# Optimization experiments

Hardware: AMD Instinct MI355X
Metric: run time of the kernel (lower is better)

Reference implementation:

```python
import jax, jax.numpy as jnp
import numpy as np

B = 4096; NINP = 512; NHID = 2048; NB = 8; BS = 256  # block_size_out
ATT_OUT = 4 * BS; TOPK = 4; DK_I = 64; NH = 4; DK_M = 16


def setup_inputs() -> dict:
    ks = jax.random.split(jax.random.key(0), 16)
    g = lambda i, shape, s=0.01: s * jax.random.normal(ks[i], shape, dtype=jnp.float32)
    return dict(
        inp=jax.random.normal(ks[0], (B, NINP), dtype=jnp.float32),
        hx=jax.random.normal(ks[1], (B, NHID), dtype=jnp.float32),
        cx=jax.random.normal(ks[2], (B, NHID), dtype=jnp.float32),
        # inp_att group-linear projections (GroupLinearLayer init 0.01*randn)
        Wq_i=g(3, (NB, BS, DK_I)), Wk_i=g(4, (2, NINP, DK_I)), Wv_i=g(5, (2, NINP, ATT_OUT)),
        # mha group-linear projections (4 heads * d_k=16)
        Wq_m=g(6, (NB, BS, NH * DK_M)), Wk_m=g(7, (NB, BS, NH * DK_M)), Wv_m=g(8, (NB, BS, NH * DK_M)),
        fc_w=g(9, (BS, NH * DK_M), 0.05), fc_b=jnp.zeros((BS,), jnp.float32),
        gate_w=g(10, (BS, NH * DK_M), 0.05), gate_b=jnp.zeros((BS,), jnp.float32),
        # blockified LSTMCell: k=NB independent (ATT_OUT -> BS) cells, gate order i,f,g,o
        Wih=g(11, (NB, 4 * BS, ATT_OUT), 0.02), Whh=g(12, (NB, 4 * BS, BS), 0.05),
        b_ih=jnp.zeros((NB, 4 * BS), jnp.float32), b_hh=jnp.zeros((NB, 4 * BS), jnp.float32),
        step=0,
    )


def _fwd(inp, hx, cx, Wq_i, Wk_i, Wv_i, Wq_m, Wk_m, Wv_m, fc_w, fc_b, gate_w, gate_b, Wih, Whh, b_ih, b_hh):
    b = inp.shape[0]
    # input read: concat null slot + input (num_blocks_in=1, num_modules_read_input=2)
    x = inp.reshape(b, 1, NINP)
    x = jnp.concatenate([jnp.zeros_like(x), x], axis=1)  # (b, 2, NINP); slot 0 = null
    hq = hx.reshape(b, NB, BS)
    q = jnp.einsum('bkd,kde->bke', hq, Wq_i)              # (b, NB, DK_I)
    k = jnp.einsum('bkd,kde->bke', x, Wk_i)               # (b, 2, DK_I)
    v = jnp.einsum('bkd,kde->bke', x, Wv_i)               # (b, 2, ATT_OUT)
    iatt = jax.nn.softmax(jnp.einsum('bqe,bke->bqk', q, k) / jnp.sqrt(jnp.float32(DK_I)), axis=-1)
    inp_use = jnp.einsum('bqk,bke->bqe', iatt, v)         # (b, NB, ATT_OUT); skip_write => identity fc
    # top-k selection: blocks with HIGHEST null-attention get frozen (masked out)
    _, botk = jax.lax.top_k(iatt[:, :, 0], NB - TOPK)
    mblk = jnp.ones((b, NB), inp.dtype).at[jnp.arange(b)[:, None], botk].set(0.0)
    mblk = jax.lax.stop_gradient(mblk)                    # mask.detach()
    mask = jnp.repeat(mblk, BS, axis=1)                   # (b, NHID)
    # block-diagonal LSTM cell (post blockify_params)
    hb = hx.reshape(b, NB, BS); cb = cx.reshape(b, NB, BS)
    gates = jnp.einsum('bkd,kgd->bkg', inp_use, Wih) + jnp.einsum('bkh,kgh->bkg', hb, Whh) + b_ih + b_hh
    ig, fg, gg, og = jnp.split(gates, 4, axis=-1)
    c_new = jax.nn.sigmoid(fg) * cb + jax.nn.sigmoid(ig) * jnp.tanh(gg)
    h_new = jax.nn.sigmoid(og) * jnp.tanh(c_new)          # (b, NB, BS)
    # step attention among blocks; blocked_grad: forward identity, backward masked
    m3 = mblk[:, :, None]
    hg = m3 * h_new + jax.lax.stop_gradient((1.0 - m3) * h_new)
    qm = jnp.einsum('bkd,kde->bke', hg, Wq_m).reshape(b, NB, NH, DK_M)
    km = jnp.einsum('bkd,kde->bke', hg, Wk_m).reshape(b, NB, NH, DK_M)
    vm = jnp.einsum('bkd,kde->bke', hg, Wv_m).reshape(b, NB, NH, DK_M)
    a = jax.nn.softmax(jnp.einsum('bqhe,bkhe->bhqk', qm, km) / jnp.sqrt(jnp.float32(DK_M)), axis=-1)
    o = jnp.einsum('bhqk,bkhe->bqhe', a, vm).reshape(b, NB, NH * DK_M)
    att_out = jax.nn.sigmoid(o @ gate_w.T + gate_b) * jnp.tanh(o @ fc_w.T + fc_b)  # residual gating
    h_new = (h_new + att_out).reshape(b, NHID)
    c_new = c_new.reshape(b, NHID)
    hx_out = mask * h_new + (1.0 - mask) * hx
    cx_out = mask * c_new + (1.0 - mask) * cx
    return hx_out, cx_out, mask


def reference(inp, hx, cx, Wq_i, Wk_i, Wv_i, Wq_m, Wk_m, Wv_m, fc_w, fc_b, gate_w, gate_b, Wih, Whh, b_ih, b_hh, step):
    return _fwd(inp, hx, cx, Wq_i, Wk_i, Wv_i, Wq_m, Wk_m, Wv_m, fc_w, fc_b, gate_w, gate_b, Wih, Whh, b_ih, b_hh)
```

## Files before the change

### kernel.cpp

```cpp
#include <hip/hip_runtime.h>
#include <hip/hip_bf16.h>


#define B_SZ 4096
#define NINP 512
#define NHID 2048
#define NB 8
#define BSZ 256
#define ATT_OUT 1024

typedef __attribute__((ext_vector_type(8))) short bf16x8;
typedef __attribute__((ext_vector_type(8))) unsigned short u16x8;
typedef __attribute__((ext_vector_type(4))) float f32x4;

__device__ __forceinline__ float sigf(float x) { return 1.0f / (1.0f + expf(-x)); }

__device__ __forceinline__ unsigned short f2bf(float x) {
    unsigned u = __float_as_uint(x);
    unsigned r = (u + 0x7fff + ((u >> 16) & 1)) >> 16;
    return (unsigned short)r;
}
__device__ __forceinline__ float bf2f(unsigned short u) {
    return __uint_as_float((unsigned)u << 16);
}

__device__ __forceinline__ void gload16(const void* g, void* l) {
    __builtin_amdgcn_global_load_lds(
        (const __attribute__((address_space(1))) unsigned int*)(unsigned long long)g,
        (__attribute__((address_space(3))) unsigned int*)(unsigned int)(unsigned long long)l,
        16, 0, 0);
}

__device__ __forceinline__ u16x8 cvt8(const float4& a, const float4& b) {
    u16x8 v;
    v[0] = f2bf(a.x); v[1] = f2bf(a.y); v[2] = f2bf(a.z); v[3] = f2bf(a.w);
    v[4] = f2bf(b.x); v[5] = f2bf(b.y); v[6] = f2bf(b.z); v[7] = f2bf(b.w);
    return v;
}

__global__ __launch_bounds__(256) void prep1_kernel(
    const float* __restrict__ gw, const float* __restrict__ fw,
    unsigned short* __restrict__ Wgfb,
    const float4* __restrict__ hx4, u16x8* __restrict__ hxb8,
    const float4* __restrict__ inp4, u16x8* __restrict__ inpb8,
    const float* __restrict__ WvSrc, unsigned short* __restrict__ Wvb)
{
    __shared__ float tile[32][33];
    const int bid = blockIdx.x;
    if (bid < 128) {
        int t = bid * 256 + threadIdx.x;
        Wgfb[t] = f2bf((t < 16384) ? gw[t] : fw[t - 16384]);
    } else if (bid < 4224) {
        long i = (long)(bid - 128) * 256 + threadIdx.x;
        hxb8[i] = cvt8(hx4[i * 2], hx4[i * 2 + 1]);
    } else if (bid < 5248) {
        long i = (long)(bid - 4224) * 256 + threadIdx.x;
        inpb8[i] = cvt8(inp4[i * 2], inp4[i * 2 + 1]);
    } else {
        const int b2 = bid - 5248;
        const int n0 = (b2 & 31) * 32;
        const int k0 = (b2 >> 5) * 32;
        const int tx = threadIdx.x & 31;
        const int ty = threadIdx.x >> 5;
        #pragma unroll
        for (int r = 0; r < 4; ++r)
            tile[ty + r * 8][tx] = WvSrc[(long)(k0 + ty + r * 8) * 1024 + n0 + tx];
        __syncthreads();
        #pragma unroll
        for (int r = 0; r < 4; ++r)
            Wvb[(long)(n0 + ty + r * 8) * 512 + k0 + tx] = f2bf(tile[tx][ty + r * 8]);
    }
}

__global__ __launch_bounds__(256) void prepW_kernel(
    const float4* __restrict__ Wih4, u16x8* __restrict__ Wihb8,
    const float4* __restrict__ Whh4, u16x8* __restrict__ Whhb8)
{
    const int bid = blockIdx.x;
    if (bid < 4096) {
        long i = (long)bid * 256 + threadIdx.x;
        Wihb8[i] = cvt8(Wih4[i * 2], Wih4[i * 2 + 1]);
    } else {
        long i = (long)(bid - 4096) * 256 + threadIdx.x;
        Whhb8[i] = cvt8(Whh4[i * 2], Whh4[i * 2 + 1]);
    }
}

__global__ __launch_bounds__(256) void qkvw_kernel(
    const float* __restrict__ Wq, const float* __restrict__ Wk,
    const float* __restrict__ Wv, unsigned short* __restrict__ out)
{
    int idx = blockIdx.x * 256 + threadIdx.x;
    int k = idx & 255;
    int n = (idx >> 8) % 192;
    int kb = idx / (192 * 256);
    const float* src = (n < 64) ? Wq : (n < 128) ? Wk : Wv;
    int nn = n & 63;
    out[idx] = f2bf(src[(long)kb * 16384 + k * 64 + nn]);
}

__global__ __launch_bounds__(256) void qk1_kernel(
    const float* __restrict__ inp, const float* __restrict__ hx,
    const float* __restrict__ Wk1, const float* __restrict__ Wq,
    float* __restrict__ k1, float* __restrict__ q)
{
    const int role = blockIdx.y;
    const int m0 = blockIdx.x * 64;
    const float* A; long lda; const float* Bw; int K; float* C; int ldc;
    if (role == 8) {
        A = inp + (long)m0 * 512; lda = 512; Bw = Wk1; K = 512;
        C = k1 + (long)m0 * 64; ldc = 64;
    } else {
        A = hx + (long)m0 * 2048 + role * 256; lda = 2048;
        Bw = Wq + (long)role * 256 * 64; K = 256;
        C = q + (long)m0 * 512 + role * 64; ldc = 512;
    }

    __shared__ float As[64][17];
    __shared__ float Bs[16][65];

    const int t = threadIdx.x;
    const int ty = t >> 4;
    const int tx = t & 15;

    float acc[4][4] = {};

    for (int k0 = 0; k0 < K; k0 += 16) {
        {
            int m = t >> 2, kk = (t & 3) << 2;
            float4 av = *reinterpret_cast<const float4*>(&A[(long)m * lda + k0 + kk]);
            As[m][kk] = av.x; As[m][kk + 1] = av.y;
            As[m][kk + 2] = av.z; As[m][kk + 3] = av.w;
        }
        {
            int kr = t >> 4, c = (t & 15) << 2;
            float4 bv = *reinterpret_cast<const float4*>(&Bw[(long)(k0 + kr) * 64 + c]);
            Bs[kr][c] = bv.x; Bs[kr][c + 1] = bv.y;
            Bs[kr][c + 2] = bv.z; Bs[kr][c + 3] = bv.w;
        }
        __syncthreads();
        #pragma unroll
        for (int kk = 0; kk < 16; ++kk) {
            float a[4], b[4];
            #pragma unroll
            for (int i = 0; i < 4; ++i) a[i] = As[ty * 4 + i][kk];
            #pragma unroll
            for (int j = 0; j < 4; ++j) b[j] = Bs[kk][tx * 4 + j];
            #pragma unroll
            for (int i = 0; i < 4; ++i)
                #pragma unroll
                for (int j = 0; j < 4; ++j) acc[i][j] += a[i] * b[j];
        }
        __syncthreads();
    }
    #pragma unroll
    for (int i = 0; i < 4; ++i) {
        float4 v = {acc[i][0], acc[i][1], acc[i][2], acc[i][3]};
        *reinterpret_cast<float4*>(&C[(long)(ty * 4 + i) * ldc + tx * 4]) = v;
    }
}

__global__ __launch_bounds__(256, 2) void gemm_mfma_bf(
    const unsigned short* __restrict__ A,
    const unsigned short* __restrict__ Bm,
    unsigned short* __restrict__ Cv,
    int K, int lda, int ldb, int ldc,
    long aOffZ, long bOffZ, long cOffZ)
{
    const int m0 = blockIdx.x * 128;
    const int n0 = blockIdx.y * 64;
    const int z = blockIdx.z;
    A += (long)z * aOffZ;
    Bm += (long)z * bOffZ;

    __shared__ unsigned short As[128 * 64];
    __shared__ unsigned short Bs[64 * 64];

    const int t = threadIdx.x;
    const int wid = t >> 6;
    const int l = t & 63;
    const int l15 = l & 15;
    const int l4 = l >> 4;
    const int wm = wid >> 1;
    const int wn = wid & 1;

    f32x4 acc[4][2];
    #pragma unroll
    for (int m = 0; m < 4; ++m)
        #pragma unroll
        for (int n = 0; n < 2; ++n)
            acc[m][n] = (f32x4){0.f, 0.f, 0.f, 0.f};

    for (int k0 = 0; k0 < K; k0 += 64) {
        #pragma unroll
        for (int s = 0; s < 4; ++s) {
            int ci = (wid * 4 + s) * 64 + l;
            int r = ci >> 3, cs = ci & 7;
            gload16(A + (long)(m0 + r) * lda + k0 + ((cs ^ (r & 7)) << 3), &As[ci * 8]);
        }
        #pragma unroll
        for (int s = 0; s < 2; ++s) {
            int ci = (wid * 2 + s) * 64 + l;
            int rn = ci >> 3, cs = ci & 7;
            gload16(Bm + (long)(n0 + rn) * ldb + k0 + ((cs ^ (rn & 7)) << 3), &Bs[ci * 8]);
        }
        __syncthreads();
        #pragma unroll
        for (int kh = 0; kh < 2; ++kh) {
            bf16x8 af[4];
            #pragma unroll
            for (int m = 0; m < 4; ++m) {
                int r = wm * 64 + m * 16 + l15;
                int c = kh * 4 + l4;
                af[m] = *reinterpret_cast<const bf16x8*>(&As[r * 64 + ((c ^ (r & 7)) << 3)]);
            }
            #pragma unroll
            for (int nf = 0; nf < 2; ++nf) {
                int rn = wn * 32 + nf * 16 + l15;
                int c = kh * 4 + l4;
                bf16x8 bf = *reinterpret_cast<const bf16x8*>(
                    &Bs[rn * 64 + ((c ^ (rn & 7)) << 3)]);
                #pragma unroll
                for (int m = 0; m < 4; ++m)
                    acc[m][nf] = __builtin_amdgcn_mfma_f32_16x16x32_bf16(
                        af[m], bf, acc[m][nf], 0, 0, 0);
            }
        }
        __syncthreads();
    }

    #pragma unroll
    for (int nf = 0; nf < 2; ++nf) {
        const int ccol = n0 + wn * 32 + nf * 16 + l15;
        #pragma unroll
        for (int m = 0; m < 4; ++m) {
            #pragma unroll
            for (int r = 0; r < 4; ++r) {
                const long crow = m0 + wm * 64 + m * 16 + l4 * 4 + r;
                Cv[(long)z * cOffZ + crow * ldc + ccol] = f2bf(acc[m][nf][r]);
            }
        }
    }
}

__global__ __launch_bounds__(256) void s1_mask_kernel(
    const float* __restrict__ q, const float* __restrict__ k1,
    float* __restrict__ w_ws, float* __restrict__ mblk,
    float* __restrict__ mask_out)
{
    const int wave = threadIdx.x >> 6;
    const int lane = threadIdx.x & 63;
    const int b = blockIdx.x * 4 + wave;

    float p[8];
    const float kv = k1[(long)b * 64 + lane];
    #pragma unroll
    for (int kb = 0; kb < 8; ++kb)
        p[kb] = q[(long)b * 512 + kb * 64 + lane] * kv;

    #pragma unroll
    for (int off = 1; off < 64; off <<= 1) {
        #pragma unroll
        for (int kb = 0; kb < 8; ++kb) p[kb] += __shfl_xor(p[kb], off);
    }

    float s[8], mv[8];
    #pragma unroll
    for (int kb = 0; kb < 8; ++kb) s[kb] = p[kb] * 0.125f;

    #pragma unroll
    for (int j = 0; j < 8; ++j) {
        int r = 0;
        #pragma unroll
        for (int i = 0; i < 8; ++i)
            r += (s[i] < s[j]) || (s[i] == s[j] && i < j);
        mv[j] = (r >= 4) ? 1.0f : 0.0f;
    }
    if (lane < 8) {
        w_ws[(long)b * 8 + lane] = sigf(s[lane]);
        mblk[(long)b * 8 + lane] = mv[lane];
    }
    #pragma unroll
    for (int it = 0; it < 8; ++it) {
        const float mvv = mv[it];
        float4 v = {mvv, mvv, mvv, mvv};
        *reinterpret_cast<float4*>(&mask_out[(long)b * 2048 + it * 256 + lane * 4]) = v;
    }
}

__global__ __launch_bounds__(256, 2) void gates_mfma_kernel(
    const unsigned short* __restrict__ Ab,
    const unsigned short* __restrict__ Hb,
    const unsigned short* __restrict__ Wihb,
    const unsigned short* __restrict__ Whhb,
    const float* __restrict__ b_ih, const float* __restrict__ b_hh,
    const float* __restrict__ w_ws, const float* __restrict__ mblk,
    const float* __restrict__ cx,
    float* __restrict__ h_out, float* __restrict__ c_out,
    unsigned short* __restrict__ hn_b)
{
    const int m0 = blockIdx.x * 128;
    const int j0 = blockIdx.y * 64;
    const int kb = blockIdx.z;

    __shared__ unsigned short As[128 * 64];
    __shared__ unsigned short Bs[256 * 64];
    __shared__ float wv[128];
    __shared__ float mbs[128];

    const int t = threadIdx.x;
    const int wid = t >> 6;
    const int l = t & 63;
    const int l15 = l & 15;
    const int l4 = l >> 4;
    const int wm = wid >> 1;
    const int wj = wid & 1;

    if (t < 128) {
        wv[t] = w_ws[(long)(m0 + t) * 8 + kb];
        mbs[t] = mblk[(long)(m0 + t) * 8 + kb];
    }

    f32x4 acc[4][8];
    #pragma unroll
    for (int m = 0; m < 4; ++m)
        #pragma unroll
        for (int n = 0; n < 8; ++n)
            acc[m][n] = (f32x4){0.f, 0.f, 0.f, 0.f};

    auto stage = [&](const unsigned short* Aptr, long lda,
                     const unsigned short* Bptr, long ldb, int k0) {
        #pragma unroll
        for (int s = 0; s < 4; ++s) {
            int ci = (wid * 4 + s) * 64 + l;
            int r = ci >> 3, cs = ci & 7;
            const unsigned short* g = Aptr + (long)r * lda + k0 + ((cs ^ (r & 7)) << 3);
            gload16(g, &As[ci * 8]);
        }
        #pragma unroll
        for (int s = 0; s < 8; ++s) {
            int ci = (wid * 8 + s) * 64 + l;
            int rn = ci >> 3, cs = ci & 7;
            int sg = rn >> 6, jl = rn & 63;
            const unsigned short* g = Bptr + (long)(sg * 256 + j0 + jl) * ldb + k0
                                      + ((cs ^ (rn & 7)) << 3);
            gload16(g, &Bs[ci * 8]);
        }
    };

    auto compute = [&]() {
        #pragma unroll
        for (int kh = 0; kh < 2; ++kh) {
            bf16x8 af[4];
            #pragma unroll
            for (int m = 0; m < 4; ++m) {
                int r = wm * 64 + m * 16 + l15;
                int c = kh * 4 + l4;
                af[m] = *reinterpret_cast<const bf16x8*>(&As[r * 64 + ((c ^ (r & 7)) << 3)]);
            }
            #pragma unroll
            for (int sg = 0; sg < 4; ++sg) {
                #pragma unroll
                for (int jf = 0; jf < 2; ++jf) {
                    int rn = sg * 64 + wj * 32 + jf * 16 + l15;
                    int c = kh * 4 + l4;
                    bf16x8 bf = *reinterpret_cast<const bf16x8*>(
                        &Bs[rn * 64 + ((c ^ (rn & 7)) << 3)]);
                    #pragma unroll
                    for (int m = 0; m < 4; ++m)
                        acc[m][sg * 2 + jf] = __builtin_amdgcn_mfma_f32_16x16x32_bf16(
                            af[m], bf, acc[m][sg * 2 + jf], 0, 0, 0);
                }
            }
        }
    };

    {
        const unsigned short* A1 = Ab + (long)m0 * 1024;
        const unsigned short* B1 = Wihb + (long)kb * 1024 * 1024;
        for (int k0 = 0; k0 < 1024; k0 += 64) {
            stage(A1, 1024, B1, 1024, k0);
            __syncthreads();
            compute();
            __syncthreads();
        }
    }

    {
        float wsc[4][4];
        #pragma unroll
        for (int m = 0; m < 4; ++m)
            #pragma unroll
            for (int r = 0; r < 4; ++r)
                wsc[m][r] = wv[wm * 64 + m * 16 + l4 * 4 + r];
        #pragma unroll
        for (int m = 0; m < 4; ++m)
            #pragma unroll
            for (int n = 0; n < 8; ++n)
                #pragma unroll
                for (int r = 0; r < 4; ++r)
                    acc[m][n][r] *= wsc[m][r];
    }

    {
        const unsigned short* A2 = Hb + (long)m0 * 2048 + kb * 256;
        const unsigned short* B2 = Whhb + (long)kb * 1024 * 256;
        for (int k0 = 0; k0 < 256; k0 += 64) {
            stage(A2, 2048, B2, 256, k0);
            __syncthreads();
            compute();
            __syncthreads();
        }
    }

    #pragma unroll
    for (int jf = 0; jf < 2; ++jf) {
        const int jcol = j0 + wj * 32 + jf * 16 + l15;
        const long bb = (long)kb * 1024 + jcol;
        const float bI = b_ih[bb] + b_hh[bb];
        const float bF = b_ih[bb + 256] + b_hh[bb + 256];
        const float bG = b_ih[bb + 512] + b_hh[bb + 512];
        const float bO = b_ih[bb + 768] + b_hh[bb + 768];
        #pragma unroll
        for (int m = 0; m < 4; ++m) {
            #pragma unroll
            for (int r = 0; r < 4; ++r) {
                const long row = m0 + wm * 64 + m * 16 + l4 * 4 + r;
                const long idx = row * 2048 + kb * 256 + jcol;
                const float mv = mbs[wm * 64 + m * 16 + l4 * 4 + r];
                const float ig = acc[m][0 + jf][r] + bI;
                const float fg = acc[m][2 + jf][r] + bF;
                const float gg = acc[m][4 + jf][r] + bG;
                const float og = acc[m][6 + jf][r] + bO;
                const float co = cx[idx];
                const float cn = sigf(fg) * co + sigf(ig) * tanhf(gg);
                const float hn = sigf(og) * tanhf(cn);
                h_out[idx] = hn;
                c_out[idx] = (mv != 0.0f) ? cn : co;
                hn_b[idx] = f2bf(hn);
            }
        }
    }
}

__global__ __launch_bounds__(256) void attn_m2_kernel(
    const unsigned short* __restrict__ qkv, unsigned short* __restrict__ ob)
{
    const int tid = blockIdx.x * 256 + threadIdx.x;
    const int b = tid >> 5;
    const int qkb = (tid >> 2) & 7;
    const int h = tid & 3;
    const unsigned short* base = qkv + (long)b * 1536;

    float qv[16];
    {
        const unsigned short* qp = base + qkb * 192 + h * 16;
        #pragma unroll
        for (int e = 0; e < 16; ++e) qv[e] = bf2f(qp[e]);
    }

    float sc[8];
    float mx = -1e30f;
    #pragma unroll
    for (int kk = 0; kk < 8; ++kk) {
        const unsigned short* kp = base + kk * 192 + 64 + h * 16;
        float s = 0.f;
        #pragma unroll
        for (int e = 0; e < 16; ++e) s += qv[e] * bf2f(kp[e]);
        s *= 0.25f;
        sc[kk] = s;
        mx = fmaxf(mx, s);
    }
    float den = 0.f;
    #pragma unroll
    for (int kk = 0; kk < 8; ++kk) { sc[kk] = expf(sc[kk] - mx); den += sc[kk]; }
    const float inv = 1.0f / den;

    float ov[16] = {};
    #pragma unroll
    for (int kk = 0; kk < 8; ++kk) {
        const float pw = sc[kk] * inv;
        const unsigned short* vp = base + kk * 192 + 128 + h * 16;
        #pragma unroll
        for (int e = 0; e < 16; ++e) ov[e] += pw * bf2f(vp[e]);
    }
    u16x8 r0, r1;
    #pragma unroll
    for (int e = 0; e < 8; ++e) { r0[e] = f2bf(ov[e]); r1[e] = f2bf(ov[e + 8]); }
    unsigned short* op = ob + (long)((b * 8 + qkb) * 64 + h * 16);
    *reinterpret_cast<u16x8*>(op) = r0;
    *reinterpret_cast<u16x8*>(op + 8) = r1;
}

__global__ __launch_bounds__(256) void attn_final_kernel(
    const unsigned short* __restrict__ ob,
    const unsigned short* __restrict__ Wgfb,
    const float* __restrict__ gate_b, const float* __restrict__ fc_b,
    const float* __restrict__ mblk,
    const float* __restrict__ hx,
    float* __restrict__ h_out)
{
    const int m0 = blockIdx.x * 128;
    const int j0 = blockIdx.y * 64;

    __shared__ unsigned short As[128 * 64];
    __shared__ unsigned short Bs[128 * 64];

    const int t = threadIdx.x;
    const int wid = t >> 6;
    const int l = t & 63;
    const int l15 = l & 15;
    const int l4 = l >> 4;
    const int wm = wid >> 1;
    const int wn = wid & 1;

    #pragma unroll
    for (int s = 0; s < 4; ++s) {
        int ci = (wid * 4 + s) * 64 + l;
        int r = ci >> 3, cs = ci & 7;
        gload16(ob + (long)(m0 + r) * 64 + ((cs ^ (r & 7)) << 3), &As[ci * 8]);
    }
    #pragma unroll
    for (int s = 0; s < 4; ++s) {
        int ci = (wid * 4 + s) * 64 + l;
        int r = ci >> 3, cs = ci & 7;
        int n = (r < 64) ? (j0 + r) : (256 + j0 + (r - 64));
        gload16(Wgfb + (long)n * 64 + ((cs ^ (r & 7)) << 3), &Bs[ci * 8]);
    }
    __syncthreads();

    f32x4 acc[4][2][2];
    #pragma unroll
    for (int m = 0; m < 4; ++m)
        #pragma unroll
        for (int nf = 0; nf < 2; ++nf)
            #pragma unroll
            for (int gf = 0; gf < 2; ++gf)
                acc[m][nf][gf] = (f32x4){0.f, 0.f, 0.f, 0.f};

    #pragma unroll
    for (int kh = 0; kh < 2; ++kh) {
        const int c = kh * 4 + l4;
        bf16x8 af[4];
        #pragma unroll
        for (int m = 0; m < 4; ++m) {
            int r = wm * 64 + m * 16 + l15;
            af[m] = *reinterpret_cast<const bf16x8*>(&As[r * 64 + ((c ^ (r & 7)) << 3)]);
        }
        #pragma unroll
        for (int nf = 0; nf < 2; ++nf) {
            int rg = wn * 32 + nf * 16 + l15;
            bf16x8 bg = *reinterpret_cast<const bf16x8*>(
                &Bs[rg * 64 + ((c ^ (rg & 7)) << 3)]);
            int rf = 64 + rg;
            bf16x8 bfv = *reinterpret_cast<const bf16x8*>(
                &Bs[rf * 64 + ((c ^ (rf & 7)) << 3)]);
            #pragma unroll
            for (int m = 0; m < 4; ++m) {
                acc[m][nf][0] = __builtin_amdgcn_mfma_f32_16x16x32_bf16(
                    af[m], bg, acc[m][nf][0], 0, 0, 0);
                acc[m][nf][1] = __builtin_amdgcn_mfma_f32_16x16x32_bf16(
                    af[m], bfv, acc[m][nf][1], 0, 0, 0);
            }
        }
    }

    #pragma unroll
    for (int nf = 0; nf < 2; ++nf) {
        const int j = j0 + wn * 32 + nf * 16 + l15;
        const float gb = gate_b[j];
        const float fb = fc_b[j];
        #pragma unroll
        for (int m = 0; m < 4; ++m) {
            #pragma unroll
            for (int r = 0; r < 4; ++r) {
                const long p = m0 + wm * 64 + m * 16 + l4 * 4 + r;
                const float g = acc[m][nf][0][r] + gb;
                const float f = acc[m][nf][1][r] + fb;
                const float att = sigf(g) * tanhf(f);
                const long idx = (p >> 3) * 2048 + (p & 7) * 256 + j;
                const float mv = mblk[p];
                const float hn = h_out[idx] + att;
                h_out[idx] = (mv != 0.0f) ? hn : hx[idx];
            }
        }
    }
}

extern "C" void kernel_launch(void* const* d_in, const int* in_sizes, int n_in,
                              void* d_out, int out_size, void* d_ws, size_t ws_size,
                              hipStream_t stream) {
    const float* inp    = (const float*)d_in[0];
    const float* hx     = (const float*)d_in[1];
    const float* cx     = (const float*)d_in[2];
    const float* Wq_i   = (const float*)d_in[3];
    const float* Wk_i   = (const float*)d_in[4];
    const float* Wv_i   = (const float*)d_in[5];
    const float* Wq_m   = (const float*)d_in[6];
    const float* Wk_m   = (const float*)d_in[7];
    const float* Wv_m   = (const float*)d_in[8];
    const float* fc_w   = (const float*)d_in[9];
    const float* fc_b   = (const float*)d_in[10];
    const float* gate_w = (const float*)d_in[11];
    const float* gate_b = (const float*)d_in[12];
    const float* Wih    = (const float*)d_in[13];
    const float* Whh    = (const float*)d_in[14];
    const float* b_ih   = (const float*)d_in[15];
    const float* b_hh   = (const float*)d_in[16];

    float* out      = (float*)d_out;
    float* h_out    = out;
    float* c_out    = out + (long)B_SZ * 2048;
    float* mask_out = out + (long)2 * B_SZ * 2048;

    float* ws   = (float*)d_ws;
    float* w_ws = ws;
    float* mblk = w_ws + (long)B_SZ * 8;
    unsigned short* v1b = (unsigned short*)(mblk + (long)B_SZ * 8);
    unsigned short* hxb = v1b + (long)B_SZ * 1024;
    unsigned short* hnb  = hxb + (long)B_SZ * 2048;
    unsigned short* Wihb = hnb + (long)B_SZ * 2048;
    unsigned short* Whhb = Wihb + (long)8 * 1024 * 1024;
    unsigned short* Wgfb = Whhb + (long)8 * 1024 * 256;
    float* k1 = (float*)Wihb;
    float* q  = k1 + (long)B_SZ * 64;
    unsigned short* inpb = (unsigned short*)(q + (long)B_SZ * 512);
    unsigned short* Wvb  = inpb + (long)B_SZ * 512;
    unsigned short* Wqkvb = Wihb;
    unsigned short* qkvb  = hxb;
    unsigned short* ob    = v1b;

    prep1_kernel<<<dim3(5760), 256, 0, stream>>>(
        gate_w, fc_w, Wgfb,
        (const float4*)hx, (u16x8*)hxb,
        (const float4*)inp, (u16x8*)inpb,
        Wv_i + (long)NINP * ATT_OUT, Wvb);
    qk1_kernel<<<dim3(64, 9), 256, 0, stream>>>(
        inp, hx, Wk_i + (long)NINP * 64, Wq_i, k1, q);
    gemm_mfma_bf<<<dim3(32, 16, 1), 256, 0, stream>>>(
        inpb, Wvb, v1b, 512, 512, 512, 1024, 0, 0, 0);
    s1_mask_kernel<<<dim3(B_SZ / 4), 256, 0, stream>>>(q, k1, w_ws, mblk, mask_out);
    prepW_kernel<<<dim3(5120), 256, 0, stream>>>(
        (const float4*)Wih, (u16x8*)Wihb, (const float4*)Whh, (u16x8*)Whhb);
    gates_mfma_kernel<<<dim3(B_SZ / 128, 4, 8), 256, 0, stream>>>(
        v1b, hxb, Wihb, Whhb, b_ih, b_hh, w_ws, mblk, cx, h_out, c_out, hnb);
    qkvw_kernel<<<dim3(1536), 256, 0, stream>>>(Wq_m, Wk_m, Wv_m, Wqkvb);
    gemm_mfma_bf<<<dim3(32, 3, 8), 256, 0, stream>>>(
        hnb, Wqkvb, qkvb, 256, 2048, 256, 1536, 256, (long)192 * 256, 192);
    attn_m2_kernel<<<dim3(B_SZ * 32 / 256), 256, 0, stream>>>(qkvb, ob);
    attn_final_kernel<<<dim3(256, 4), 256, 0, stream>>>(
        ob, Wgfb, gate_b, fc_b, mblk, hx, h_out);
}
```

Baseline: 288.0 us.

## Drop fp32 h_out round trip, remap gates blocks, enlarge qk1 tiles

The gates kernel no longer writes fp32 h_new to h_out. The final attention kernel now reads the bf16 hn buffer instead, which removes a 32 MB fp32 write and a 32 MB fp32 read. The gates grid is remapped so consecutive workgroups fall on different kb blocks, likely to spread L2/XCD traffic. qk1 now uses 128-row tiles with 8x4 accumulators per thread. Reading h_new from bf16 lowers the precision of the residual add in the output.

```diff
diff --git a/kernel.cpp b/kernel.cpp
--- a/kernel.cpp
+++ b/kernel.cpp
@@ -105,7 +105,7 @@
     float* __restrict__ k1, float* __restrict__ q)
 {
     const int role = blockIdx.y;
-    const int m0 = blockIdx.x * 64;
+    const int m0 = blockIdx.x * 128;
     const float* A; long lda; const float* Bw; int K; float* C; int ldc;
     if (role == 8) {
         A = inp + (long)m0 * 512; lda = 512; Bw = Wk1; K = 512;
@@ -116,18 +116,20 @@
         C = q + (long)m0 * 512 + role * 64; ldc = 512;
     }
 
-    __shared__ float As[64][17];
+    __shared__ float As[128][17];
     __shared__ float Bs[16][65];
 
     const int t = threadIdx.x;
     const int ty = t >> 4;
     const int tx = t & 15;
 
-    float acc[4][4] = {};
+    float acc[8][4] = {};
 
     for (int k0 = 0; k0 < K; k0 += 16) {
-        {
-            int m = t >> 2, kk = (t & 3) << 2;
+        #pragma unroll
+        for (int u = 0; u < 2; ++u) {
+            int slot = t + 256 * u;
+            int m = slot >> 2, kk = (slot & 3) << 2;
             float4 av = *reinterpret_cast<const float4*>(&A[(long)m * lda + k0 + kk]);
             As[m][kk] = av.x; As[m][kk + 1] = av.y;
             As[m][kk + 2] = av.z; As[m][kk + 3] = av.w;
@@ -141,22 +143,22 @@
         __syncthreads();
         #pragma unroll
         for (int kk = 0; kk < 16; ++kk) {
-            float a[4], b[4];
-            #pragma unroll
-            for (int i = 0; i < 4; ++i) a[i] = As[ty * 4 + i][kk];
+            float a[8], b[4];
+            #pragma unroll
+            for (int i = 0; i < 8; ++i) a[i] = As[ty * 8 + i][kk];
             #pragma unroll
             for (int j = 0; j < 4; ++j) b[j] = Bs[kk][tx * 4 + j];
             #pragma unroll
-            for (int i = 0; i < 4; ++i)
+            for (int i = 0; i < 8; ++i)
                 #pragma unroll
                 for (int j = 0; j < 4; ++j) acc[i][j] += a[i] * b[j];
         }
         __syncthreads();
     }
     #pragma unroll
-    for (int i = 0; i < 4; ++i) {
+    for (int i = 0; i < 8; ++i) {
         float4 v = {acc[i][0], acc[i][1], acc[i][2], acc[i][3]};
-        *reinterpret_cast<float4*>(&C[(long)(ty * 4 + i) * ldc + tx * 4]) = v;
+        *reinterpret_cast<float4*>(&C[(long)(ty * 8 + i) * ldc + tx * 4]) = v;
     }
 }
 
@@ -296,12 +298,14 @@
     const float* __restrict__ b_ih, const float* __restrict__ b_hh,
     const float* __restrict__ w_ws, const float* __restrict__ mblk,
     const float* __restrict__ cx,
-    float* __restrict__ h_out, float* __restrict__ c_out,
+    float* __restrict__ c_out,
     unsigned short* __restrict__ hn_b)
 {
-    const int m0 = blockIdx.x * 128;
-    const int j0 = blockIdx.y * 64;
-    const int kb = blockIdx.z;
+    const int n = blockIdx.x + 32 * blockIdx.y + 128 * blockIdx.z;
+    const int w = (n & 7) * 128 + (n >> 3);
+    const int m0 = (w & 31) * 128;
+    const int j0 = ((w >> 5) & 3) * 64;
+    const int kb = w >> 7;
 
     __shared__ unsigned short As[128 * 64];
     __shared__ unsigned short Bs[256 * 64];
@@ -325,8 +329,8 @@
     #pragma unroll
     for (int m = 0; m < 4; ++m)
         #pragma unroll
-        for (int n = 0; n < 8; ++n)
-            acc[m][n] = (f32x4){0.f, 0.f, 0.f, 0.f};
+        for (int nn = 0; nn < 8; ++nn)
+            acc[m][nn] = (f32x4){0.f, 0.f, 0.f, 0.f};
 
     auto stage = [&](const unsigned short* Aptr, long lda,
                      const unsigned short* Bptr, long ldb, int k0) {
@@ -396,10 +400,10 @@
         #pragma unroll
         for (int m = 0; m < 4; ++m)
             #pragma unroll
-            for (int n = 0; n < 8; ++n)
+            for (int nn = 0; nn < 8; ++nn)
                 #pragma unroll
                 for (int r = 0; r < 4; ++r)
-                    acc[m][n][r] *= wsc[m][r];
+                    acc[m][nn][r] *= wsc[m][r];
     }
 
     {
@@ -435,7 +439,6 @@
                 const float co = cx[idx];
                 const float cn = sigf(fg) * co + sigf(ig) * tanhf(gg);
                 const float hn = sigf(og) * tanhf(cn);
-                h_out[idx] = hn;
                 c_out[idx] = (mv != 0.0f) ? cn : co;
                 hn_b[idx] = f2bf(hn);
             }
@@ -498,6 +501,7 @@
     const float* __restrict__ gate_b, const float* __restrict__ fc_b,
     const float* __restrict__ mblk,
     const float* __restrict__ hx,
+    const unsigned short* __restrict__ hnb,
     float* __restrict__ h_out)
 {
     const int m0 = blockIdx.x * 128;
@@ -580,7 +584,7 @@
                 const float att = sigf(g) * tanhf(f);
                 const long idx = (p >> 3) * 2048 + (p & 7) * 256 + j;
                 const float mv = mblk[p];
-                const float hn = h_out[idx] + att;
+                const float hn = bf2f(hnb[idx]) + att;
                 h_out[idx] = (mv != 0.0f) ? hn : hx[idx];
             }
         }
@@ -635,7 +639,7 @@
         (const float4*)hx, (u16x8*)hxb,
         (const float4*)inp, (u16x8*)inpb,
         Wv_i + (long)NINP * ATT_OUT, Wvb);
-    qk1_kernel<<<dim3(64, 9), 256, 0, stream>>>(
+    qk1_kernel<<<dim3(32, 9), 256, 0, stream>>>(
         inp, hx, Wk_i + (long)NINP * 64, Wq_i, k1, q);
     gemm_mfma_bf<<<dim3(32, 16, 1), 256, 0, stream>>>(
         inpb, Wvb, v1b, 512, 512, 512, 1024, 0, 0, 0);
@@ -643,11 +647,11 @@
     prepW_kernel<<<dim3(5120), 256, 0, stream>>>(
         (const float4*)Wih, (u16x8*)Wihb, (const float4*)Whh, (u16x8*)Whhb);
     gates_mfma_kernel<<<dim3(B_SZ / 128, 4, 8), 256, 0, stream>>>(
-        v1b, hxb, Wihb, Whhb, b_ih, b_hh, w_ws, mblk, cx, h_out, c_out, hnb);
+        v1b, hxb, Wihb, Whhb, b_ih, b_hh, w_ws, mblk, cx, c_out, hnb);
     qkvw_kernel<<<dim3(1536), 256, 0, stream>>>(Wq_m, Wk_m, Wv_m, Wqkvb);
     gemm_mfma_bf<<<dim3(32, 3, 8), 256, 0, stream>>>(
         hnb, Wqkvb, qkvb, 256, 2048, 256, 1536, 256, (long)192 * 256, 192);
     attn_m2_kernel<<<dim3(B_SZ * 32 / 256), 256, 0, stream>>>(qkvb, ob);
     attn_final_kernel<<<dim3(256, 4), 256, 0, stream>>>(
-        ob, Wgfb, gate_b, fc_b, mblk, hx, h_out);
-}
+        ob, Wgfb, gate_b, fc_b, mblk, hx, hnb, h_out);
+}
```

Measured after the change: 284.6 us. Within noise of the previous version (-1.2%).
